# Kernel tuning notes

Measured on AMD Instinct MI355X. Metric: run time of the kernel, lower is better.

## Reference

```python
import jax, jax.numpy as jnp
import numpy as np

B, T, D, U = 64, 512, 1024, 128


def setup_inputs() -> dict:
    key = jax.random.key(0)
    k1, k2, k3, k4, k5 = jax.random.split(key, 5)
    x = jax.random.normal(k1, (B, T, D), dtype=jnp.float32)
    mask = jnp.ones((B, T), dtype=jnp.int32)
    # learned parameters (glorot-ish scale for kernel)
    kernel = jax.random.normal(k2, (D, U), dtype=jnp.float32) * (1.0 / np.sqrt(D))
    bias = jnp.zeros((U,), dtype=jnp.float32)
    left_boundary = jax.random.normal(k3, (U,), dtype=jnp.float32) * 0.1
    right_boundary = jax.random.normal(k4, (U,), dtype=jnp.float32) * 0.1
    return {"x": x, "mask": mask, "kernel": kernel, "bias": bias,
            "left_boundary": left_boundary, "right_boundary": right_boundary}


def _shift_right(m):  # [B,T,1] -> pad one zero step at front along time
    return jnp.concatenate([jnp.zeros_like(m[:, :1]), m[:, :-1]], axis=1)


def _shift_left(m):  # [B,T,1] -> pad one zero step at end along time
    return jnp.concatenate([m[:, 1:], jnp.zeros_like(m[:, :1])], axis=1)


def reference(x, mask, kernel, bias, left_boundary, right_boundary):
    # input energy: linear activation of dense projection  [B,T,U]
    energy = jnp.einsum('btd,du->btu', x, kernel) + bias
    # boundary energies with mask (faithful to source semantics)
    m = mask.astype(energy.dtype)[:, :, None]                     # [B,T,1]
    start_mask = (m > _shift_right(m)).astype(energy.dtype)       # first valid step
    end_mask = (_shift_left(m) > m).astype(energy.dtype)          # as written in source
    energy = energy + start_mask * left_boundary[None, None, :]
    energy = energy + end_mask * right_boundary[None, None, :]
    return energy
```

## Files before the change

kernel.cpp:

```cpp
#include <hip/hip_runtime.h>

#define BB 64
#define TT 512
#define DD 1024
#define UU 128
#define MM (BB * TT)
#define BK 64
#define NCHUNK (DD / BK)
#define LDA 72
#define LDB 72

typedef short short8 __attribute__((ext_vector_type(8)));
typedef float f32x4 __attribute__((ext_vector_type(4)));

__device__ __forceinline__ unsigned short f2bf(float f) {
    union { float f; unsigned u; } v; v.f = f;
    unsigned u = v.u;
    return (unsigned short)((u + 0x7fffu + ((u >> 16) & 1u)) >> 16);
}

__global__ __launch_bounds__(256) void wprep_kernel(const float* __restrict__ w,
                                                    unsigned short* __restrict__ wt) {
    int tg = blockIdx.x * 256 + threadIdx.x;
    int kg = tg & 7;
    int n  = (tg >> 3) & 127;
    int kc = tg >> 10;
    union { unsigned short s[8]; uint4 v; } o;
#pragma unroll
    for (int j = 0; j < 8; ++j) {
        int k = kc * 64 + kg * 8 + j;
        o.s[j] = f2bf(w[k * 128 + n]);
    }
    *(uint4*)(wt + tg * 8) = o.v;
}

__global__ __launch_bounds__(256, 2) void crf_energy_kernel(
    const float* __restrict__ x,
    const int* __restrict__ mask,
    const unsigned short* __restrict__ wt,
    const float* __restrict__ bias,
    const float* __restrict__ lb,
    const float* __restrict__ rb,
    float* __restrict__ out)
{
    __shared__ unsigned short lA[64 * LDA];
    __shared__ unsigned short lB[128 * LDB];

    const int tid  = threadIdx.x;
    const int wave = tid >> 6;
    const int lane = tid & 63;
    const int q    = lane >> 4;
    const int r    = lane & 15;
    const int row0 = blockIdx.x * 64;

    const int mhalf = wave >> 1;
    const int nhalf = wave & 1;

    f32x4 acc[2][4];
#pragma unroll
    for (int i = 0; i < 2; ++i)
#pragma unroll
        for (int j = 0; j < 4; ++j) acc[i][j] = (f32x4){0.f, 0.f, 0.f, 0.f};

    for (int kc = 0; kc < NCHUNK; ++kc) {
#pragma unroll
        for (int p = 0; p < 4; ++p) {
            int c  = p * 256 + tid;
            int m  = c >> 4;
            int kg = c & 15;
            const float4 v = *(const float4*)(x + (size_t)(row0 + m) * DD + kc * BK + kg * 4);
            union { unsigned short s[4]; unsigned long long u; } pk;
            pk.s[0] = f2bf(v.x); pk.s[1] = f2bf(v.y);
            pk.s[2] = f2bf(v.z); pk.s[3] = f2bf(v.w);
            *(unsigned long long*)(&lA[m * LDA + kg * 4]) = pk.u;
        }
#pragma unroll
        for (int p = 0; p < 4; ++p) {
            int c  = p * 256 + tid;
            int n  = c >> 3;
            int kg = c & 7;
            uint4 v = *(const uint4*)(wt + (size_t)kc * 8192 + n * 64 + kg * 8);
            *(uint4*)(&lB[n * LDB + kg * 8]) = v;
        }
        __syncthreads();

#pragma unroll
        for (int ks = 0; ks < 2; ++ks) {
            short8 a[2], b[4];
#pragma unroll
            for (int mt = 0; mt < 2; ++mt)
                a[mt] = *(const short8*)(&lA[(mhalf * 32 + mt * 16 + r) * LDA + ks * 32 + q * 8]);
#pragma unroll
            for (int nt = 0; nt < 4; ++nt)
                b[nt] = *(const short8*)(&lB[(nhalf * 64 + nt * 16 + r) * LDB + ks * 32 + q * 8]);
#pragma unroll
            for (int mt = 0; mt < 2; ++mt)
#pragma unroll
                for (int nt = 0; nt < 4; ++nt)
                    acc[mt][nt] = __builtin_amdgcn_mfma_f32_16x16x32_bf16(
                        a[mt], b[nt], acc[mt][nt], 0, 0, 0);
        }
        __syncthreads();
    }

#pragma unroll
    for (int mt = 0; mt < 2; ++mt) {
#pragma unroll
        for (int nt = 0; nt < 4; ++nt) {
            const int n = nhalf * 64 + nt * 16 + r;
            const float bi = bias[n];
            const float lbn = lb[n];
            const float rbn = rb[n];
#pragma unroll
            for (int reg = 0; reg < 4; ++reg) {
                const int m = row0 + mhalf * 32 + mt * 16 + q * 4 + reg;
                const int t = m & (TT - 1);
                const int cur  = mask[m];
                const int prev = (t != 0)      ? mask[m - 1] : 0;
                const int nxt  = (t != TT - 1) ? mask[m + 1] : 0;
                float e = acc[mt][nt][reg] + bi;
                if (cur > prev) e += lbn;
                if (nxt > cur)  e += rbn;
                out[(size_t)m * UU + n] = e;
            }
        }
    }
}

extern "C" void kernel_launch(void* const* d_in, const int* in_sizes, int n_in,
                              void* d_out, int out_size, void* d_ws, size_t ws_size,
                              hipStream_t stream) {
    const float* x    = (const float*)d_in[0];
    const int*   mask = (const int*)d_in[1];
    const float* w    = (const float*)d_in[2];
    const float* bias = (const float*)d_in[3];
    const float* lb   = (const float*)d_in[4];
    const float* rb   = (const float*)d_in[5];
    float* out = (float*)d_out;
    unsigned short* wt = (unsigned short*)d_ws;

    wprep_kernel<<<64, 256, 0, stream>>>(w, wt);
    crf_energy_kernel<<<512, 256, 0, stream>>>(x, mask, wt, bias, lb, rb, out);
}
```

Measured before the change: 231.8 us.

## Drop LDS staging; load A and B fragments directly into registers with prefetch

The GEMM kernel no longer stages x and the bf16 weights through shared memory. Each wave loads its own x rows straight from global memory into registers, converts them to bf16, and prefetches the next K-chunk while it computes. It reads B fragments directly from global memory, which should mostly hit in L2 given the small weight matrix. Blocks shrink to 32 rows with 1024 blocks and launch bounds of 4, removing __syncthreads and LDS traffic and raising occupancy. The cost is that each block now reads the weights from global memory and the x reads are less coalesced per lane.

```diff
diff --git a/kernel.cpp b/kernel.cpp
--- a/kernel.cpp
+++ b/kernel.cpp
@@ -1,14 +1,9 @@
 #include <hip/hip_runtime.h>
 
-#define BB 64
 #define TT 512
 #define DD 1024
 #define UU 128
-#define MM (BB * TT)
-#define BK 64
-#define NCHUNK (DD / BK)
-#define LDA 72
-#define LDB 72
+#define MM 32768
 
 typedef short short8 __attribute__((ext_vector_type(8)));
 typedef float f32x4 __attribute__((ext_vector_type(4)));
@@ -34,7 +29,7 @@
     *(uint4*)(wt + tg * 8) = o.v;
 }
 
-__global__ __launch_bounds__(256, 2) void crf_energy_kernel(
+__global__ __launch_bounds__(256, 4) void crf_energy_kernel(
     const float* __restrict__ x,
     const int* __restrict__ mask,
     const unsigned short* __restrict__ wt,
@@ -43,86 +38,90 @@
     const float* __restrict__ rb,
     float* __restrict__ out)
 {
-    __shared__ unsigned short lA[64 * LDA];
-    __shared__ unsigned short lB[128 * LDB];
-
     const int tid  = threadIdx.x;
     const int wave = tid >> 6;
     const int lane = tid & 63;
     const int q    = lane >> 4;
     const int r    = lane & 15;
-    const int row0 = blockIdx.x * 64;
 
-    const int mhalf = wave >> 1;
-    const int nhalf = wave & 1;
+    const int mt   = wave >> 1;
+    const int nh   = wave & 1;
+    const int row0 = blockIdx.x * 32 + mt * 16;
 
-    f32x4 acc[2][4];
+    const float* __restrict__ xrow = x + (size_t)(row0 + r) * DD;
+    const unsigned short* __restrict__ wbase = wt + (size_t)(nh * 64 + r) * 64 + q * 8;
+
+    f32x4 acc[4];
 #pragma unroll
-    for (int i = 0; i < 2; ++i)
+    for (int nt = 0; nt < 4; ++nt) acc[nt] = (f32x4){0.f, 0.f, 0.f, 0.f};
+
+    float4 araw[2][2];
 #pragma unroll
-        for (int j = 0; j < 4; ++j) acc[i][j] = (f32x4){0.f, 0.f, 0.f, 0.f};
+    for (int ks = 0; ks < 2; ++ks) {
+        const float* p = xrow + ks * 32 + q * 8;
+        araw[ks][0] = *(const float4*)(p);
+        araw[ks][1] = *(const float4*)(p + 4);
+    }
 
-    for (int kc = 0; kc < NCHUNK; ++kc) {
+#pragma unroll 2
+    for (int kc = 0; kc < 16; ++kc) {
+        const int kcn = (kc < 15) ? kc + 1 : kc;
+        float4 anxt[2][2];
 #pragma unroll
-        for (int p = 0; p < 4; ++p) {
-            int c  = p * 256 + tid;
-            int m  = c >> 4;
-            int kg = c & 15;
-            const float4 v = *(const float4*)(x + (size_t)(row0 + m) * DD + kc * BK + kg * 4);
-            union { unsigned short s[4]; unsigned long long u; } pk;
-            pk.s[0] = f2bf(v.x); pk.s[1] = f2bf(v.y);
-            pk.s[2] = f2bf(v.z); pk.s[3] = f2bf(v.w);
-            *(unsigned long long*)(&lA[m * LDA + kg * 4]) = pk.u;
+        for (int ks = 0; ks < 2; ++ks) {
+            const float* p = xrow + kcn * 64 + ks * 32 + q * 8;
+            anxt[ks][0] = *(const float4*)(p);
+            anxt[ks][1] = *(const float4*)(p + 4);
         }
+
+        short8 afrag[2];
 #pragma unroll
-        for (int p = 0; p < 4; ++p) {
-            int c  = p * 256 + tid;
-            int n  = c >> 3;
-            int kg = c & 7;
-            uint4 v = *(const uint4*)(wt + (size_t)kc * 8192 + n * 64 + kg * 8);
-            *(uint4*)(&lB[n * LDB + kg * 8]) = v;
+        for (int ks = 0; ks < 2; ++ks) {
+            union { unsigned short s[8]; short8 v; } pk;
+            pk.s[0] = f2bf(araw[ks][0].x); pk.s[1] = f2bf(araw[ks][0].y);
+            pk.s[2] = f2bf(araw[ks][0].z); pk.s[3] = f2bf(araw[ks][0].w);
+            pk.s[4] = f2bf(araw[ks][1].x); pk.s[5] = f2bf(araw[ks][1].y);
+            pk.s[6] = f2bf(araw[ks][1].z); pk.s[7] = f2bf(araw[ks][1].w);
+            afrag[ks] = pk.v;
         }
-        __syncthreads();
+
+        const unsigned short* wkc = wbase + (size_t)kc * 8192;
+#pragma unroll
+        for (int ks = 0; ks < 2; ++ks) {
+            short8 b[4];
+#pragma unroll
+            for (int nt = 0; nt < 4; ++nt)
+                b[nt] = *(const short8*)(wkc + nt * 1024 + ks * 32);
+#pragma unroll
+            for (int nt = 0; nt < 4; ++nt)
+                acc[nt] = __builtin_amdgcn_mfma_f32_16x16x32_bf16(
+                    afrag[ks], b[nt], acc[nt], 0, 0, 0);
+        }
 
 #pragma unroll
         for (int ks = 0; ks < 2; ++ks) {
-            short8 a[2], b[4];
-#pragma unroll
-            for (int mt = 0; mt < 2; ++mt)
-                a[mt] = *(const short8*)(&lA[(mhalf * 32 + mt * 16 + r) * LDA + ks * 32 + q * 8]);
-#pragma unroll
-            for (int nt = 0; nt < 4; ++nt)
-                b[nt] = *(const short8*)(&lB[(nhalf * 64 + nt * 16 + r) * LDB + ks * 32 + q * 8]);
-#pragma unroll
-            for (int mt = 0; mt < 2; ++mt)
-#pragma unroll
-                for (int nt = 0; nt < 4; ++nt)
-                    acc[mt][nt] = __builtin_amdgcn_mfma_f32_16x16x32_bf16(
-                        a[mt], b[nt], acc[mt][nt], 0, 0, 0);
+            araw[ks][0] = anxt[ks][0];
+            araw[ks][1] = anxt[ks][1];
         }
-        __syncthreads();
     }
 
 #pragma unroll
-    for (int mt = 0; mt < 2; ++mt) {
+    for (int nt = 0; nt < 4; ++nt) {
+        const int n = nh * 64 + nt * 16 + r;
+        const float bi  = bias[n];
+        const float lbn = lb[n];
+        const float rbn = rb[n];
 #pragma unroll
-        for (int nt = 0; nt < 4; ++nt) {
-            const int n = nhalf * 64 + nt * 16 + r;
-            const float bi = bias[n];
-            const float lbn = lb[n];
-            const float rbn = rb[n];
-#pragma unroll
-            for (int reg = 0; reg < 4; ++reg) {
-                const int m = row0 + mhalf * 32 + mt * 16 + q * 4 + reg;
-                const int t = m & (TT - 1);
-                const int cur  = mask[m];
-                const int prev = (t != 0)      ? mask[m - 1] : 0;
-                const int nxt  = (t != TT - 1) ? mask[m + 1] : 0;
-                float e = acc[mt][nt][reg] + bi;
-                if (cur > prev) e += lbn;
-                if (nxt > cur)  e += rbn;
-                out[(size_t)m * UU + n] = e;
-            }
+        for (int reg = 0; reg < 4; ++reg) {
+            const int m = row0 + q * 4 + reg;
+            const int t = m & (TT - 1);
+            const int cur  = mask[m];
+            const int prev = (t != 0)      ? mask[m - 1] : 0;
+            const int nxt  = (t != TT - 1) ? mask[m + 1] : 0;
+            float e = acc[nt][reg] + bi;
+            if (cur > prev) e += lbn;
+            if (nxt > cur)  e += rbn;
+            out[(size_t)m * UU + n] = e;
         }
     }
 }
@@ -140,5 +139,5 @@
     unsigned short* wt = (unsigned short*)d_ws;
 
     wprep_kernel<<<64, 256, 0, stream>>>(w, wt);
-    crf_energy_kernel<<<512, 256, 0, stream>>>(x, mask, wt, bias, lb, rb, out);
+    crf_energy_kernel<<<1024, 256, 0, stream>>>(x, mask, wt, bias, lb, rb, out);
 }
```

Result: slower. 254.4 us (+9.7%).
